# Kernel optimization log

Measured on AMD Instinct MI355X. Metric: run time of the kernel, lower is better.

The kernel has to match this reference:

```python
import jax, jax.numpy as jnp
import numpy as np

BIN_SIZE = 128
DIST_MULT = 0.1
CLIP_LOW = 0.0
LN_EPS = 1e-6


def setup_inputs() -> dict:
    key = jax.random.key(0)
    ks = jax.random.split(key, 16)
    B, N, F = 8, 12800, 256
    D, H = 128, 256          # distance_dim, hidden_dim
    MAX_BINS = 200
    s = lambda k, shape: jax.random.normal(k, shape, dtype=jnp.float32) * 0.05
    return {
        "x": jax.random.normal(ks[0], (B, N, F), dtype=jnp.float32),
        "msk": jnp.ones((B, N), dtype=bool),
        "rotations": jax.random.normal(ks[1], (D, MAX_BINS // 2), dtype=jnp.float32),
        "ln_gamma": jnp.ones((F,), dtype=jnp.float32),
        "ln_beta": jnp.zeros((F,), dtype=jnp.float32),
        "w0": s(ks[2], (F, H)), "b0": jnp.zeros((H,), jnp.float32),
        "w1": s(ks[3], (H, H)), "b1": jnp.zeros((H,), jnp.float32),
        "w2": s(ks[4], (H, D)), "b2": jnp.zeros((D,), jnp.float32),
        "W_t": s(ks[5], (F, F)), "b_t": jnp.zeros((F,), jnp.float32),
        "W_h": s(ks[6], (F, F)),
        "theta": s(ks[7], (F, F)),
    }


def _forward(x, msk, rotations, ln_gamma, ln_beta, w0, b0, w1, b1, w2, b2,
             W_t, b_t, W_h, theta):
    B, N, F = x.shape
    n_bins = N // BIN_SIZE

    # LayerNormalization(axis=-1, epsilon=1e-6)
    mu = jnp.mean(x, axis=-1, keepdims=True)
    var = jnp.var(x, axis=-1, keepdims=True)
    xn = (x - mu) * jax.lax.rsqrt(var + LN_EPS) * ln_gamma + ln_beta

    # ffn_dist: two elu hidden layers + linear output to distance_dim
    h = jax.nn.elu(xn @ w0 + b0)
    h = jax.nn.elu(h @ w1 + b1)
    x_dist = h @ w2 + b2                                   # [B, N, D]

    # LSH binning: project, argmax over signed projections, argsort into bins
    mul = x_dist @ rotations[:, : n_bins // 2]             # [B, N, n_bins/2]
    cmul = jnp.concatenate([mul, -mul], axis=-1)           # [B, N, n_bins]
    bin_idx = jnp.argmax(cmul, axis=-1) + jnp.where(~msk, n_bins - 1, 0)
    bins_split = jnp.argsort(bin_idx, axis=-1).reshape(B, n_bins, BIN_SIZE)
    flat = bins_split.reshape(B, N)

    def take(a):  # gather with batch_dims=1, then split into bins
        return jnp.take_along_axis(a, flat[..., None], axis=1).reshape(
            B, n_bins, BIN_SIZE, a.shape[-1])

    x_msg_b = take(x_dist)                                 # [B, nb, bs, D]
    x_feat_b = take(xn)                                    # [B, nb, bs, F]
    msk_b = take(msk.astype(x.dtype)[..., None])           # [B, nb, bs, 1]

    # NodePairGaussianKernel on each bin
    na = jnp.sum(x_msg_b * x_msg_b, axis=-1)               # [B, nb, bs]
    d2 = (na[..., :, None] - 2.0 * jnp.einsum('bnif,bnjf->bnij', x_msg_b, x_msg_b)
          + na[..., None, :])
    dm = jnp.exp(-DIST_MULT * jnp.sqrt(jnp.maximum(d2, 1e-6)))
    dm = jnp.clip(dm, CLIP_LOW, 1.0)
    m = msk_b[..., 0]
    dm = dm * m[..., :, None] * m[..., None, :]            # [B, nb, bs, bs]

    # GHConvDense message passing (normalize_degrees=True, elu)
    in_deg = jnp.clip(jnp.sum(jnp.abs(dm), axis=-1), 0.0, 1000.0)
    norm = ((in_deg + 1e-6) ** -0.5)[..., None] * msk_b    # [B, nb, bs, 1]
    xm = x_feat_b * msk_b
    f_hom = (xm @ theta) * msk_b
    f_hom = jnp.einsum('bnij,bnjf->bnif', dm, f_hom * norm) * norm
    f_het = xm @ W_h
    gate = jax.nn.sigmoid(x_feat_b @ W_t + b_t)
    out = jax.nn.elu(gate * f_hom + (1.0 - gate) * f_het) * msk_b

    # reverse_lsh: scatter binned points back to original order
    pts = out.reshape(B, N, F)
    enc = jnp.zeros_like(pts).at[jnp.arange(B)[:, None], flat].set(pts)
    return enc


def reference(x, msk, rotations, ln_gamma, ln_beta, w0, b0, w1, b1, w2, b2,
              W_t, b_t, W_h, theta):
    return _forward(x, msk, rotations, ln_gamma, ln_beta, w0, b0, w1, b1,
                    w2, b2, W_t, b_t, W_h, theta)
```

## Files before the change

kernel.cpp:

```cpp
#include <hip/hip_runtime.h>


#define Bc   8
#define Nc   12800
#define Fc   256
#define Dc   128
#define NBINS 100
#define NBH  50
#define NPB  64
#define SPLT2 16384
#define TIE_TAU 1.0e-3f
#define FLAG_CAP 16384

typedef __attribute__((ext_vector_type(8))) short short8v;
typedef __attribute__((ext_vector_type(8))) _Float16 half8v;
typedef __attribute__((ext_vector_type(4))) _Float16 half4v;
typedef __attribute__((ext_vector_type(4))) float f32x4;

__device__ __forceinline__ float eluf(float v) { return v > 0.f ? v : __expf(v) - 1.f; }
__device__ __forceinline__ unsigned short f2bf(float f) {
  unsigned u = __float_as_uint(f);
  unsigned r = (u + 0x7FFFu + ((u >> 16) & 1u)) >> 16;
  return (unsigned short)r;
}
__device__ __forceinline__ float bf2f(unsigned short h) {
  return __uint_as_float((unsigned)h << 16);
}
__device__ __forceinline__ void split2(float v, _Float16 h[2]) {
  h[0] = (_Float16)v;
  h[1] = (_Float16)((v - (float)h[0]) * 2048.f);
}
#define C1 (1.f/2048.f)

__global__ void k0_prep(const float* __restrict__ theta, const float* __restrict__ Wh,
                        const float* __restrict__ Wt, const float* __restrict__ w0,
                        const float* __restrict__ w1, const float* __restrict__ w2,
                        const float* __restrict__ rot,
                        unsigned short* __restrict__ wcat, _Float16* __restrict__ w0s,
                        _Float16* __restrict__ w1s, _Float16* __restrict__ w2s,
                        _Float16* __restrict__ rots, int* __restrict__ flag_cnt)
{
  const int k = blockIdx.x, n = threadIdx.x;
  if (k == 0 && n == 0) *flag_cnt = 0;
  for (int nn = n; nn < 768; nn += 256) {
    const int sel = nn >> 8, f = nn & 255;
    const float* W = sel == 0 ? theta : (sel == 1 ? Wh : Wt);
    wcat[(size_t)nn*256 + k] = f2bf(W[k*256 + f]);
  }
  _Float16 h[2];
  split2(w0[k*256 + n], h);
#pragma unroll
  for (int s = 0; s < 2; ++s) w0s[s*65536 + n*256 + k] = h[s];
  split2(w1[k*256 + n], h);
#pragma unroll
  for (int s = 0; s < 2; ++s) w1s[s*65536 + n*256 + k] = h[s];
  if (n < 128) {
    split2(w2[k*128 + n], h);
#pragma unroll
    for (int s = 0; s < 2; ++s) w2s[s*32768 + n*256 + k] = h[s];
  }
  if (k < 128 && n < 112) {
    const float v = (n < NBINS) ? rot[k*100 + n] : 0.f;
    split2(v, h);
#pragma unroll
    for (int s = 0; s < 2; ++s) rots[s*14336 + n*128 + k] = h[s];
  }
}

template<int RT, int NT, int KS, int NSTR>
__device__ __forceinline__ void gemm3(const _Float16* __restrict__ sAb,
    const _Float16* __restrict__ B, int ldb, int bsplit, int n0, int lr, int lk,
    f32x4 aM[RT][NT], f32x4 aC1[RT][NT])
{
#pragma unroll
  for (int ks = 0; ks < KS; ++ks) {
    half8v a[2][RT], b[2][NT];
#pragma unroll
    for (int s = 0; s < 2; ++s) {
#pragma unroll
      for (int rt = 0; rt < RT; ++rt)
        a[s][rt] = *(const half8v*)&sAb[s*SPLT2 + (ks*4 + lk)*(NPB*8) + (rt*16 + lr)*8];
#pragma unroll
      for (int nt = 0; nt < NT; ++nt)
        b[s][nt] = *(const half8v*)&B[s*bsplit + (n0 + nt*NSTR + lr)*ldb + ks*32 + lk*8];
    }
#pragma unroll
    for (int rt = 0; rt < RT; ++rt)
#pragma unroll
      for (int nt = 0; nt < NT; ++nt) {
        aM[rt][nt]  = __builtin_amdgcn_mfma_f32_16x16x32_f16(a[0][rt], b[0][nt], aM[rt][nt], 0,0,0);
        aC1[rt][nt] = __builtin_amdgcn_mfma_f32_16x16x32_f16(a[0][rt], b[1][nt], aC1[rt][nt],0,0,0);
        aC1[rt][nt] = __builtin_amdgcn_mfma_f32_16x16x32_f16(a[1][rt], b[0][nt], aC1[rt][nt],0,0,0);
      }
  }
}

__global__ __launch_bounds__(512, 2) void k1_mfma(
    const float* __restrict__ x, const float* __restrict__ gamma, const float* __restrict__ beta,
    const _Float16* __restrict__ w0s, const _Float16* __restrict__ w1s,
    const _Float16* __restrict__ w2s, const _Float16* __restrict__ rots,
    const float* __restrict__ b0, const float* __restrict__ b1, const float* __restrict__ b2,
    unsigned short* __restrict__ xn_out, unsigned short* __restrict__ xd_out,
    int* __restrict__ bin_out, int* __restrict__ flag_cnt, int* __restrict__ flag_list)
{
  __shared__ __align__(16) _Float16 sA4[2*SPLT2];

  const int t = threadIdx.x;
  const int w = t >> 6, l = t & 63;
  const int lr = l & 15, lk = l >> 4;
  const int pt0 = blockIdx.x * NPB;

  {
    const int r = t >> 3, c8 = t & 7;
    const float* xr = x + (size_t)(pt0 + r)*Fc + c8*32;
    float4 xv[8];
    float s1 = 0.f, s2 = 0.f;
#pragma unroll
    for (int i = 0; i < 8; ++i) {
      xv[i] = *(const float4*)&xr[i*4];
      s1 += xv[i].x + xv[i].y + xv[i].z + xv[i].w;
      s2 += xv[i].x*xv[i].x + xv[i].y*xv[i].y + xv[i].z*xv[i].z + xv[i].w*xv[i].w;
    }
    s1 += __shfl_xor(s1, 1); s2 += __shfl_xor(s2, 1);
    s1 += __shfl_xor(s1, 2); s2 += __shfl_xor(s2, 2);
    s1 += __shfl_xor(s1, 4); s2 += __shfl_xor(s2, 4);
    const float mu = s1 * (1.f/256.f);
    const float var = s2 * (1.f/256.f) - mu*mu;
    const float rs = 1.f / sqrtf(var + 1e-6f);
#pragma unroll
    for (int i = 0; i < 8; ++i) {
      const int c = c8*32 + i*4;
      const float4 g  = *(const float4*)&gamma[c];
      const float4 be = *(const float4*)&beta[c];
      float v[4] = { (xv[i].x-mu)*rs*g.x + be.x, (xv[i].y-mu)*rs*g.y + be.y,
                     (xv[i].z-mu)*rs*g.z + be.z, (xv[i].w-mu)*rs*g.w + be.w };
      ushort4 ov; _Float16 h[4][2];
#pragma unroll
      for (int e = 0; e < 4; ++e) split2(v[e], h[e]);
      ov.x = f2bf(v[0]); ov.y = f2bf(v[1]); ov.z = f2bf(v[2]); ov.w = f2bf(v[3]);
      *(ushort4*)&xn_out[(size_t)(pt0 + r)*Fc + c] = ov;
      const int off = (c >> 3)*(NPB*8) + r*8 + (c & 7);
#pragma unroll
      for (int s = 0; s < 2; ++s) {
        half4v hv; hv[0]=h[0][s]; hv[1]=h[1][s]; hv[2]=h[2][s]; hv[3]=h[3][s];
        *(half4v*)&sA4[s*SPLT2 + off] = hv;
      }
    }
  }
  __syncthreads();

#pragma unroll 1
  for (int layer = 0; layer < 2; ++layer) {
    const _Float16* Bw = layer ? w1s : w0s;
    const float*    bb = layer ? b1  : b0;
    f32x4 aM[4][2], aC1[4][2];
#pragma unroll
    for (int rt = 0; rt < 4; ++rt)
#pragma unroll
      for (int nt = 0; nt < 2; ++nt) {
        aM[rt][nt] = (f32x4){0,0,0,0}; aC1[rt][nt] = (f32x4){0,0,0,0};
      }
    gemm3<4,2,8,16>(sA4, Bw, 256, 65536, w*32, lr, lk, aM, aC1);
    float vals[4][2][4];
#pragma unroll
    for (int nt = 0; nt < 2; ++nt) {
      const float bias = bb[w*32 + nt*16 + lr];
#pragma unroll
      for (int rt = 0; rt < 4; ++rt)
#pragma unroll
        for (int rr = 0; rr < 4; ++rr)
          vals[rt][nt][rr] = eluf(aM[rt][nt][rr] + aC1[rt][nt][rr]*C1 + bias);
    }
    __syncthreads();
#pragma unroll
    for (int nt = 0; nt < 2; ++nt) {
      const int col = w*32 + nt*16 + lr;
      const int base = (col >> 3)*(NPB*8) + (col & 7);
#pragma unroll
      for (int rt = 0; rt < 4; ++rt)
#pragma unroll
        for (int rr = 0; rr < 4; ++rr) {
          const int row = rt*16 + lk*4 + rr;
          _Float16 h[2]; split2(vals[rt][nt][rr], h);
          const int off = base + row*8;
          sA4[off] = h[0]; sA4[SPLT2 + off] = h[1];
        }
    }
    __syncthreads();
  }

  {
    f32x4 aM[4][1], aC1[4][1];
#pragma unroll
    for (int rt = 0; rt < 4; ++rt) { aM[rt][0] = (f32x4){0,0,0,0}; aC1[rt][0] = (f32x4){0,0,0,0}; }
    gemm3<4,1,8,16>(sA4, w2s, 256, 32768, w*16, lr, lk, aM, aC1);
    float vals[4][4];
    const int col = w*16 + lr;
    const float bias = b2[col];
#pragma unroll
    for (int rt = 0; rt < 4; ++rt)
#pragma unroll
      for (int rr = 0; rr < 4; ++rr) {
        const float v = aM[rt][0][rr] + aC1[rt][0][rr]*C1 + bias;
        vals[rt][rr] = v;
        xd_out[(size_t)(pt0 + rt*16 + lk*4 + rr)*Dc + col] = f2bf(v);
      }
    __syncthreads();
    {
      const int base = (col >> 3)*(NPB*8) + (col & 7);
#pragma unroll
      for (int rt = 0; rt < 4; ++rt)
#pragma unroll
        for (int rr = 0; rr < 4; ++rr) {
          const int row = rt*16 + lk*4 + rr;
          _Float16 h[2]; split2(vals[rt][rr], h);
          const int off = base + row*8;
          sA4[off] = h[0]; sA4[SPLT2 + off] = h[1];
        }
    }
    __syncthreads();
  }

  {
    float pv[4][4];
    if (w < 7) {
      f32x4 aM[4][1], aC1[4][1];
#pragma unroll
      for (int rt = 0; rt < 4; ++rt) { aM[rt][0] = (f32x4){0,0,0,0}; aC1[rt][0] = (f32x4){0,0,0,0}; }
      gemm3<4,1,4,16>(sA4, rots, 128, 14336, w*16, lr, lk, aM, aC1);
#pragma unroll
      for (int rt = 0; rt < 4; ++rt)
#pragma unroll
        for (int rr = 0; rr < 4; ++rr)
          pv[rt][rr] = aM[rt][0][rr] + aC1[rt][0][rr]*C1;
    }
    float* sMul = (float*)sA4;
    __syncthreads();
    if (w < 7) {
#pragma unroll
      for (int rt = 0; rt < 4; ++rt)
#pragma unroll
        for (int rr = 0; rr < 4; ++rr)
          sMul[(rt*16 + lk*4 + rr)*116 + w*16 + lr] = pv[rt][rr];
    }
    __syncthreads();
    if (t < NPB) {
      float best = -3.0e38f, second = -3.0e38f; int bi = 0;
      for (int j = 0; j < NBINS; ++j) {
        const float v = (j < NBH) ? sMul[t*116 + j] : -sMul[t*116 + (j - NBH)];
        if (v > best) { second = best; best = v; bi = j; }
        else if (v > second) second = v;
      }
      bin_out[pt0 + t] = bi;
      if (best - second < TIE_TAU) {
        const int slot = atomicAdd(flag_cnt, 1);
        if (slot < FLAG_CAP) flag_list[slot] = pt0 + t;
      }
    }
  }
}

__global__ __launch_bounds__(256) void k1b_repair(
    const float* __restrict__ x, const float* __restrict__ gamma, const float* __restrict__ beta,
    const float* __restrict__ w0, const float* __restrict__ b0,
    const float* __restrict__ w1, const float* __restrict__ b1,
    const float* __restrict__ w2, const float* __restrict__ b2,
    const float* __restrict__ rot,
    const int* __restrict__ flag_cnt, const int* __restrict__ flag_list,
    int* __restrict__ bin_out)
{
  const int n = min(*flag_cnt, FLAG_CAP);
  __shared__ float s0[256], s1[256], rs1[4], rs2[4];
  const int t = threadIdx.x;

  for (int it = blockIdx.x; it < n; it += gridDim.x) {
    const int p = flag_list[it];
    const float xv = x[(size_t)p*Fc + t];
    float a1 = xv, a2 = xv*xv;
#pragma unroll
    for (int o = 1; o < 64; o <<= 1) { a1 += __shfl_xor(a1, o); a2 += __shfl_xor(a2, o); }
    if ((t & 63) == 0) { rs1[t>>6] = a1; rs2[t>>6] = a2; }
    __syncthreads();
    const float S1 = rs1[0]+rs1[1]+rs1[2]+rs1[3];
    const float S2 = rs2[0]+rs2[1]+rs2[2]+rs2[3];
    const float mu = S1 * (1.f/256.f);
    const float var = S2 * (1.f/256.f) - mu*mu;
    const float rsv = 1.f / sqrtf(var + 1e-6f);
    s0[t] = (xv - mu) * rsv * gamma[t] + beta[t];
    __syncthreads();
    float acc = 0.f;
    for (int k = 0; k < 256; ++k) acc += s0[k] * w0[k*256 + t];
    const float h0v = eluf(acc + b0[t]);
    __syncthreads(); s1[t] = h0v; __syncthreads();
    acc = 0.f;
    for (int k = 0; k < 256; ++k) acc += s1[k] * w1[k*256 + t];
    const float h1v = eluf(acc + b1[t]);
    __syncthreads(); s0[t] = h1v; __syncthreads();
    if (t < 128) {
      acc = 0.f;
      for (int k = 0; k < 256; ++k) acc += s0[k] * w2[k*128 + t];
      s1[t] = acc + b2[t];
    }
    __syncthreads();
    if (t < NBINS) {
      float m = 0.f;
      for (int d = 0; d < 128; ++d) m += s1[d] * rot[d*100 + t];
      s0[t] = m;
    }
    __syncthreads();
    if (t == 0) {
      float best = -3.0e38f; int bi = 0;
      for (int j = 0; j < NBINS; ++j) {
        const float v = (j < NBH) ? s0[j] : -s0[j - NBH];
        if (v > best) { best = v; bi = j; }
      }
      bin_out[p] = bi;
    }
    __syncthreads();
  }
}

__global__ __launch_bounds__(256) void k2_sort(const int* __restrict__ bin_idx,
                                               int* __restrict__ flat)
{
  __shared__ unsigned int hist[NBINS][256];
  __shared__ unsigned int off[NBINS];
  const int b = blockIdx.x, t = threadIdx.x;
  for (int i = t; i < NBINS*256; i += 256) ((unsigned int*)hist)[i] = 0u;
  __syncthreads();
  const int* bi = bin_idx + b*Nc;
  const int start = t * 50;
  for (int i = 0; i < 50; ++i) hist[bi[start+i]][t]++;
  __syncthreads();
  for (int bb = t; bb < NBINS; bb += 256) {
    unsigned run = 0;
    for (int q = 0; q < 256; ++q) { const unsigned v = hist[bb][q]; hist[bb][q] = run; run += v; }
    off[bb] = run;
  }
  __syncthreads();
  if (t == 0) {
    unsigned run = 0;
    for (int q = 0; q < NBINS; ++q) { const unsigned v = off[q]; off[q] = run; run += v; }
  }
  __syncthreads();
  int* fo = flat + b*Nc;
  for (int i = 0; i < 50; ++i) {
    const int idx = start + i;
    const int bb = bi[idx];
    fo[off[bb] + hist[bb][t]++] = idx;
  }
}

#define SXD 136

__global__ __launch_bounds__(512, 2) void k3_bins(
    const unsigned short* __restrict__ xn, const unsigned short* __restrict__ xd,
    const int* __restrict__ flat, const unsigned short* __restrict__ wcat,
    const float* __restrict__ bt, float* __restrict__ out)
{
  __shared__ __align__(16) unsigned short s_buf[128*SXD];
  __shared__ __align__(16) unsigned short s_gt[32*SXD];
  __shared__ int   s_idx[128];
  __shared__ float s_na[128];
  __shared__ float s_norm[128];

  const int t = threadIdx.x;
  const int l = t & 63, w = t >> 6;
  const int lr = l & 15, lk = l >> 4;
  const int b = blockIdx.x / NBINS, bin = blockIdx.x % NBINS;
  const int base = b * Nc;

  if (t < 128) s_idx[t] = flat[base + bin*128 + t];
  __syncthreads();

  {
    const int r0 = t >> 4, c = t & 15;
    for (int r = r0; r < 128; r += 32) {
      const unsigned short* src = xd + (size_t)(base + s_idx[r])*Dc + c*8;
      *(short8v*)&s_buf[r*SXD + c*8] = *(const short8v*)src;
    }
  }
  __syncthreads();
  if (t < 128) {
    float s = 0.f;
    for (int c = 0; c < 16; ++c) {
      short8v v = *(short8v*)&s_buf[t*SXD + c*8];
#pragma unroll
      for (int e = 0; e < 8; ++e) { const float f = bf2f((unsigned short)v[e]); s += f*f; }
    }
    s_na[t] = s;
  }
  __syncthreads();

  {
    f32x4 dot[8];
    short8v a[4];
    const int arow = w*16 + lr;
#pragma unroll
    for (int kg = 0; kg < 4; ++kg)
      a[kg] = *(short8v*)&s_buf[arow*SXD + kg*32 + lk*8];
#pragma unroll
    for (int tj = 0; tj < 8; ++tj) {
      const int brow = tj*16 + lr;
      f32x4 acc = {0.f, 0.f, 0.f, 0.f};
#pragma unroll
      for (int kg = 0; kg < 4; ++kg) {
        short8v bv = *(short8v*)&s_buf[brow*SXD + kg*32 + lk*8];
        acc = __builtin_amdgcn_mfma_f32_16x16x32_bf16(a[kg], bv, acc, 0, 0, 0);
      }
      dot[tj] = acc;
    }
    __syncthreads();
#pragma unroll
    for (int tj = 0; tj < 8; ++tj) {
      const int jj = tj*16 + lr;
      const float naj = s_na[jj];
#pragma unroll
      for (int r = 0; r < 4; ++r) {
        const int ii = w*16 + lk*4 + r;
        const float d2 = s_na[ii] + naj - 2.f*dot[tj][r];
        s_buf[ii*SXD + jj] = f2bf(__expf(-0.1f * sqrtf(fmaxf(d2, 1e-6f))));
      }
    }
  }
  __syncthreads();
  if (t < 128) {
    float s = 0.f;
    for (int c = 0; c < 16; ++c) {
      short8v v = *(short8v*)&s_buf[t*SXD + c*8];
#pragma unroll
      for (int e = 0; e < 8; ++e) s += bf2f((unsigned short)v[e]);
    }
    s = fminf(fmaxf(s, 0.f), 1000.f);
    s_norm[t] = 1.f / sqrtf(s + 1e-6f);
  }
  __syncthreads();

  const size_t xrow = (size_t)(base + s_idx[w*16 + lr]) * Fc;

  for (int ch = 0; ch < 8; ++ch) {
    const int f0 = ch * 32;
    float hg_h[2][4], hg_g[2][4];
    short8v A[8];
#pragma unroll
    for (int kg = 0; kg < 8; ++kg)
      A[kg] = *(const short8v*)&xn[xrow + kg*32 + lk*8];
#pragma unroll
    for (int tf = 0; tf < 2; ++tf) {
      const int f = f0 + tf*16 + lr;
      const unsigned short* bp = wcat + (size_t)f*256 + lk*8;
      const unsigned short* bh = wcat + (size_t)(256 + f)*256 + lk*8;
      const unsigned short* bg = wcat + (size_t)(512 + f)*256 + lk*8;
      f32x4 tacc = {0.f,0.f,0.f,0.f}, hacc = {0.f,0.f,0.f,0.f}, gacc = {0.f,0.f,0.f,0.f};
#pragma unroll
      for (int kg = 0; kg < 8; ++kg) {
        short8v bv = *(const short8v*)(bp + kg*32);
        tacc = __builtin_amdgcn_mfma_f32_16x16x32_bf16(A[kg], bv, tacc, 0, 0, 0);
        short8v hv = *(const short8v*)(bh + kg*32);
        hacc = __builtin_amdgcn_mfma_f32_16x16x32_bf16(A[kg], hv, hacc, 0, 0, 0);
        short8v gv = *(const short8v*)(bg + kg*32);
        gacc = __builtin_amdgcn_mfma_f32_16x16x32_bf16(A[kg], gv, gacc, 0, 0, 0);
      }
#pragma unroll
      for (int r = 0; r < 4; ++r) {
        const int j = w*16 + lk*4 + r;
        s_gt[(tf*16 + lr)*SXD + j] = f2bf(tacc[r] * s_norm[j]);
        hg_h[tf][r] = hacc[r];
        hg_g[tf][r] = gacc[r];
      }
    }
    __syncthreads();
    {
      const int irow = w*16 + lr;
#pragma unroll
      for (int tf = 0; tf < 2; ++tf) {
        const int f = f0 + tf*16 + lr;
        f32x4 facc = {0.f, 0.f, 0.f, 0.f};
#pragma unroll
        for (int kg = 0; kg < 4; ++kg) {
          short8v ad  = *(short8v*)&s_buf[irow*SXD + kg*32 + lk*8];
          short8v bgt = *(short8v*)&s_gt[(tf*16 + lr)*SXD + kg*32 + lk*8];
          facc = __builtin_amdgcn_mfma_f32_16x16x32_bf16(ad, bgt, facc, 0, 0, 0);
        }
        const float btf = bt[f];
#pragma unroll
        for (int r = 0; r < 4; ++r) {
          const int i = w*16 + lk*4 + r;
          const float fh = facc[r] * s_norm[i];
          const float g  = 1.f / (1.f + __expf(-(hg_g[tf][r] + btf)));
          const float val = g * fh + (1.f - g) * hg_h[tf][r];
          out[(size_t)(base + s_idx[i])*Fc + f] = eluf(val);
        }
      }
    }
    __syncthreads();
  }
}

extern "C" void kernel_launch(void* const* d_in, const int* in_sizes, int n_in,
                              void* d_out, int out_size, void* d_ws, size_t ws_size,
                              hipStream_t stream)
{
  const float* x     = (const float*)d_in[0];
  const float* rot   = (const float*)d_in[2];
  const float* gamma = (const float*)d_in[3];
  const float* beta  = (const float*)d_in[4];
  const float* w0    = (const float*)d_in[5];
  const float* b0    = (const float*)d_in[6];
  const float* w1    = (const float*)d_in[7];
  const float* b1    = (const float*)d_in[8];
  const float* w2    = (const float*)d_in[9];
  const float* b2    = (const float*)d_in[10];
  const float* Wt    = (const float*)d_in[11];
  const float* bt    = (const float*)d_in[12];
  const float* Wh    = (const float*)d_in[13];
  const float* theta = (const float*)d_in[14];
  float* out = (float*)d_out;

  char* ws = (char*)d_ws;
  unsigned short* xn   = (unsigned short*)ws;
  unsigned short* xd   = (unsigned short*)(ws + 52428800);
  int* binv            = (int*)(ws + 78643200);
  int* flat            = (int*)(ws + 79052800);
  unsigned short* wcat = (unsigned short*)(ws + 79462400);
  _Float16* w0s        = (_Float16*)(ws + 79855616);
  _Float16* w1s        = (_Float16*)(ws + 80117760);
  _Float16* w2s        = (_Float16*)(ws + 80379904);
  _Float16* rots       = (_Float16*)(ws + 80510976);
  int* fcnt            = (int*)(ws + 80568320);
  int* flist           = (int*)(ws + 80568448);

  k0_prep<<<dim3(256), dim3(256), 0, stream>>>(theta, Wh, Wt, w0, w1, w2, rot,
                                               wcat, w0s, w1s, w2s, rots, fcnt);
  k1_mfma<<<dim3((Bc*Nc)/NPB), dim3(512), 0, stream>>>(
      x, gamma, beta, w0s, w1s, w2s, rots, b0, b1, b2, xn, xd, binv, fcnt, flist);
  k1b_repair<<<dim3(2048), dim3(256), 0, stream>>>(
      x, gamma, beta, w0, b0, w1, b1, w2, b2, rot, fcnt, flist, binv);
  k2_sort<<<dim3(Bc), dim3(256), 0, stream>>>(binv, flat);
  k3_bins<<<dim3(Bc*NBINS), dim3(512), 0, stream>>>(
      xn, xd, flat, wcat, bt, out);
}
```

Baseline: 684.0 us.

## Hoist W_h and gate matmuls out of binned kernel into per-point pass

Adds a kernel that computes the heterogeneous projection and sigmoid gate for every point in original order, writing (1-g)*f_het into the output and the gate as bf16 to a workspace buffer. The binned kernel then computes only the theta projection and the dm message pass, reading the gate and partial result through the gathered indices. This moves two of the three per-bin weight GEMMs into a dense, coalesced pass. The cost is extra global traffic for the gate and a read-modify-write of the output, and the new path runs only when the workspace is large enough.

After: 578.3 us. -15.4%, faster.

```diff
diff --git a/kernel.cpp b/kernel.cpp
--- a/kernel.cpp
+++ b/kernel.cpp
@@ -11,6 +11,7 @@
 #define SPLT2 16384
 #define TIE_TAU 1.0e-3f
 #define FLAG_CAP 16384
+#define WS_NEED 133062784ULL
 
 typedef __attribute__((ext_vector_type(8))) short short8v;
 typedef __attribute__((ext_vector_type(8))) _Float16 half8v;
@@ -351,7 +352,193 @@
   }
 }
 
+__global__ __launch_bounds__(256) void k1g_hg(
+    const unsigned short* __restrict__ xn, const unsigned short* __restrict__ wcat,
+    const float* __restrict__ bt, float* __restrict__ out,
+    unsigned short* __restrict__ gatebuf)
+{
+  __shared__ __align__(16) unsigned short sX[32*256];
+  const int t = threadIdx.x;
+  const int w = t >> 6, l = t & 63;
+  const int lr = l & 15, lk = l >> 4;
+  const int pt0 = blockIdx.x * 32;
+
+  {
+    const int r = t >> 3, c8 = t & 7;
+    const unsigned short* src = xn + (size_t)(pt0 + r)*Fc + c8*32;
+#pragma unroll
+    for (int i = 0; i < 4; ++i) {
+      const int c = c8*32 + i*8;
+      *(short8v*)&sX[(c >> 3)*256 + r*8] = *(const short8v*)(src + i*8);
+    }
+  }
+  __syncthreads();
+
+#pragma unroll 1
+  for (int cs = 0; cs < 4; ++cs) {
+    const int f0 = w*64 + cs*16;
+    f32x4 hacc[2], gacc[2];
+#pragma unroll
+    for (int rt = 0; rt < 2; ++rt) { hacc[rt] = (f32x4){0,0,0,0}; gacc[rt] = (f32x4){0,0,0,0}; }
+    const unsigned short* bh = wcat + (size_t)(256 + f0 + lr)*256 + lk*8;
+    const unsigned short* bg = wcat + (size_t)(512 + f0 + lr)*256 + lk*8;
+#pragma unroll
+    for (int ks = 0; ks < 8; ++ks) {
+      short8v a0 = *(const short8v*)&sX[(ks*4 + lk)*256 + (lr)*8];
+      short8v a1 = *(const short8v*)&sX[(ks*4 + lk)*256 + (16 + lr)*8];
+      short8v bhv = *(const short8v*)(bh + ks*32);
+      short8v bgv = *(const short8v*)(bg + ks*32);
+      hacc[0] = __builtin_amdgcn_mfma_f32_16x16x32_bf16(a0, bhv, hacc[0], 0, 0, 0);
+      hacc[1] = __builtin_amdgcn_mfma_f32_16x16x32_bf16(a1, bhv, hacc[1], 0, 0, 0);
+      gacc[0] = __builtin_amdgcn_mfma_f32_16x16x32_bf16(a0, bgv, gacc[0], 0, 0, 0);
+      gacc[1] = __builtin_amdgcn_mfma_f32_16x16x32_bf16(a1, bgv, gacc[1], 0, 0, 0);
+    }
+    const int f = f0 + lr;
+    const float btf = bt[f];
+#pragma unroll
+    for (int rt = 0; rt < 2; ++rt)
+#pragma unroll
+      for (int rr = 0; rr < 4; ++rr) {
+        const int p = pt0 + rt*16 + lk*4 + rr;
+        const float g = 1.f / (1.f + __expf(-(gacc[rt][rr] + btf)));
+        out[(size_t)p*Fc + f] = (1.f - g) * hacc[rt][rr];
+        gatebuf[(size_t)p*Fc + f] = f2bf(g);
+      }
+  }
+}
+
 #define SXD 136
+
+__global__ __launch_bounds__(512, 2) void k3_hoist(
+    const unsigned short* __restrict__ xn, const unsigned short* __restrict__ xd,
+    const int* __restrict__ flat, const unsigned short* __restrict__ wcat,
+    const unsigned short* __restrict__ gatebuf, float* __restrict__ out)
+{
+  __shared__ __align__(16) unsigned short s_xd[128*SXD];
+  __shared__ __align__(16) unsigned short s_dm[128*SXD];
+  __shared__ __align__(16) unsigned short s_gt[32*SXD];
+  __shared__ int   s_idx[128];
+  __shared__ float s_na[128];
+  __shared__ float s_norm[128];
+
+  const int t = threadIdx.x;
+  const int l = t & 63, w = t >> 6;
+  const int lr = l & 15, lk = l >> 4;
+  const int b = blockIdx.x / NBINS, bin = blockIdx.x % NBINS;
+  const int base = b * Nc;
+
+  if (t < 128) s_idx[t] = flat[base + bin*128 + t];
+  __syncthreads();
+
+  {
+    const int r0 = t >> 4, c = t & 15;
+    for (int r = r0; r < 128; r += 32) {
+      const unsigned short* src = xd + (size_t)(base + s_idx[r])*Dc + c*8;
+      *(short8v*)&s_xd[r*SXD + c*8] = *(const short8v*)src;
+    }
+  }
+  __syncthreads();
+  if (t < 128) {
+    float s = 0.f;
+    for (int c = 0; c < 16; ++c) {
+      short8v v = *(short8v*)&s_xd[t*SXD + c*8];
+#pragma unroll
+      for (int e = 0; e < 8; ++e) { const float f = bf2f((unsigned short)v[e]); s += f*f; }
+    }
+    s_na[t] = s;
+  }
+  __syncthreads();
+
+  {
+    short8v a[4];
+    const int arow = w*16 + lr;
+#pragma unroll
+    for (int kg = 0; kg < 4; ++kg)
+      a[kg] = *(short8v*)&s_xd[arow*SXD + kg*32 + lk*8];
+#pragma unroll 1
+    for (int tj = 0; tj < 8; ++tj) {
+      const int brow = tj*16 + lr;
+      f32x4 acc = {0.f, 0.f, 0.f, 0.f};
+#pragma unroll
+      for (int kg = 0; kg < 4; ++kg) {
+        short8v bv = *(short8v*)&s_xd[brow*SXD + kg*32 + lk*8];
+        acc = __builtin_amdgcn_mfma_f32_16x16x32_bf16(a[kg], bv, acc, 0, 0, 0);
+      }
+      const int jj = tj*16 + lr;
+      const float naj = s_na[jj];
+#pragma unroll
+      for (int r = 0; r < 4; ++r) {
+        const int ii = w*16 + lk*4 + r;
+        const float d2 = s_na[ii] + naj - 2.f*acc[r];
+        s_dm[ii*SXD + jj] = f2bf(__expf(-0.1f * sqrtf(fmaxf(d2, 1e-6f))));
+      }
+    }
+  }
+  __syncthreads();
+  if (t < 128) {
+    float s = 0.f;
+    for (int c = 0; c < 16; ++c) {
+      short8v v = *(short8v*)&s_dm[t*SXD + c*8];
+#pragma unroll
+      for (int e = 0; e < 8; ++e) s += bf2f((unsigned short)v[e]);
+    }
+    s = fminf(fmaxf(s, 0.f), 1000.f);
+    s_norm[t] = 1.f / sqrtf(s + 1e-6f);
+  }
+  __syncthreads();
+
+  const size_t xrow = (size_t)(base + s_idx[w*16 + lr]) * Fc;
+
+#pragma unroll 1
+  for (int ch = 0; ch < 8; ++ch) {
+    const int f0 = ch * 32;
+    short8v A[8];
+#pragma unroll
+    for (int kg = 0; kg < 8; ++kg)
+      A[kg] = *(const short8v*)&xn[xrow + kg*32 + lk*8];
+#pragma unroll
+    for (int tf = 0; tf < 2; ++tf) {
+      const int f = f0 + tf*16 + lr;
+      const unsigned short* bp = wcat + (size_t)f*256 + lk*8;
+      f32x4 tacc = {0.f,0.f,0.f,0.f};
+#pragma unroll
+      for (int kg = 0; kg < 8; ++kg) {
+        short8v bv = *(const short8v*)(bp + kg*32);
+        tacc = __builtin_amdgcn_mfma_f32_16x16x32_bf16(A[kg], bv, tacc, 0, 0, 0);
+      }
+#pragma unroll
+      for (int r = 0; r < 4; ++r) {
+        const int j = w*16 + lk*4 + r;
+        s_gt[(tf*16 + lr)*SXD + j] = f2bf(tacc[r] * s_norm[j]);
+      }
+    }
+    __syncthreads();
+    {
+      const int irow = w*16 + lr;
+#pragma unroll
+      for (int tf = 0; tf < 2; ++tf) {
+        const int f = f0 + tf*16 + lr;
+        f32x4 facc = {0.f, 0.f, 0.f, 0.f};
+#pragma unroll
+        for (int kg = 0; kg < 4; ++kg) {
+          short8v ad  = *(short8v*)&s_dm[irow*SXD + kg*32 + lk*8];
+          short8v bgt = *(short8v*)&s_gt[(tf*16 + lr)*SXD + kg*32 + lk*8];
+          facc = __builtin_amdgcn_mfma_f32_16x16x32_bf16(ad, bgt, facc, 0, 0, 0);
+        }
+#pragma unroll
+        for (int r = 0; r < 4; ++r) {
+          const int i = w*16 + lk*4 + r;
+          const size_t orow = (size_t)(base + s_idx[i]) * Fc + f;
+          const float fh = facc[r] * s_norm[i];
+          const float g  = bf2f(gatebuf[orow]);
+          const float partial = out[orow];
+          out[orow] = eluf(g * fh + partial);
+        }
+      }
+    }
+    __syncthreads();
+  }
+}
 
 __global__ __launch_bounds__(512, 2) void k3_bins(
     const unsigned short* __restrict__ xn, const unsigned short* __restrict__ xd,
@@ -372,7 +559,6 @@
 
   if (t < 128) s_idx[t] = flat[base + bin*128 + t];
   __syncthreads();
-
   {
     const int r0 = t >> 4, c = t & 15;
     for (int r = r0; r < 128; r += 32) {
@@ -391,7 +577,6 @@
     s_na[t] = s;
   }
   __syncthreads();
-
   {
     f32x4 dot[8];
     short8v a[4];
@@ -437,7 +622,7 @@
   __syncthreads();
 
   const size_t xrow = (size_t)(base + s_idx[w*16 + lr]) * Fc;
-
+#pragma unroll 1
   for (int ch = 0; ch < 8; ++ch) {
     const int f0 = ch * 32;
     float hg_h[2][4], hg_g[2][4];
@@ -529,6 +714,9 @@
   _Float16* rots       = (_Float16*)(ws + 80510976);
   int* fcnt            = (int*)(ws + 80568320);
   int* flist           = (int*)(ws + 80568448);
+  unsigned short* gate = (unsigned short*)(ws + 80633984);
+
+  const bool hoist = (ws_size >= WS_NEED);
 
   k0_prep<<<dim3(256), dim3(256), 0, stream>>>(theta, Wh, Wt, w0, w1, w2, rot,
                                                wcat, w0s, w1s, w2s, rots, fcnt);
@@ -537,6 +725,12 @@
   k1b_repair<<<dim3(2048), dim3(256), 0, stream>>>(
       x, gamma, beta, w0, b0, w1, b1, w2, b2, rot, fcnt, flist, binv);
   k2_sort<<<dim3(Bc), dim3(256), 0, stream>>>(binv, flat);
-  k3_bins<<<dim3(Bc*NBINS), dim3(512), 0, stream>>>(
-      xn, xd, flat, wcat, bt, out);
-}
+  if (hoist) {
+    k1g_hg<<<dim3((Bc*Nc)/32), dim3(256), 0, stream>>>(xn, wcat, bt, out, gate);
+    k3_hoist<<<dim3(Bc*NBINS), dim3(512), 0, stream>>>(
+        xn, xd, flat, wcat, gate, out);
+  } else {
+    k3_bins<<<dim3(Bc*NBINS), dim3(512), 0, stream>>>(
+        xn, xd, flat, wcat, bt, out);
+  }
+}
```
